# Kernel optimization log

Measured on AMD Instinct MI355X. Metric: run time of the kernel, lower is better.

## Reference

```python
import jax, jax.numpy as jnp
import numpy as np

B, N = 8, 2048
DIN, DH, DE = 32, 64, 64
R = 3          # number_relations
L = 3          # num_layers -> 1 first + 1 block + 1 last
PRED_IN = DH * (L - 1) + DE  # concat: 64*2 + 64 = 192
EPS_BN = 1e-5
EPS_NORM = 1e-12


def setup_inputs() -> dict:
    key = jax.random.key(0)
    ks = jax.random.split(key, 12)
    x = jax.random.normal(ks[0], (B, N, DIN), jnp.float32)
    # relation labels in {0..R}; 0 = no edge, 1..R = relation type
    relation = jax.random.randint(ks[1], (B, N, N), 0, R + 1).astype(jnp.int32)
    # adjacency is the 0/1 edge indicator (float), as the torch code treats it
    adj = (relation > 0).astype(jnp.float32)
    s = 0.05
    w_first = jax.random.normal(ks[2], (R, DIN, DH), jnp.float32) * s
    b_first = jnp.zeros((DH,), jnp.float32)
    w_block = jax.random.normal(ks[3], (R, DH, DH), jnp.float32) * s
    b_block = jnp.zeros((DH,), jnp.float32)
    w_last = jax.random.normal(ks[4], (R, DH, DE), jnp.float32) * s
    b_last = jnp.zeros((DE,), jnp.float32)
    w_map = jax.random.normal(ks[5], (PRED_IN, DE), jnp.float32) * s
    b_map = jnp.zeros((DE,), jnp.float32)
    return {"x": x, "relation": relation, "adj": adj,
            "w_first": w_first, "b_first": b_first,
            "w_block": w_block, "b_block": b_block,
            "w_last": w_last, "b_last": b_last,
            "w_map": w_map, "b_map": b_map}


def _graph_conv(x, rel, W, b):
    # rel: [B,N,N] (int labels or float adjacency); W: [R, din, dout]
    y = jnp.zeros((x.shape[0], x.shape[1], W.shape[2]), x.dtype)
    for i in range(R):  # fixed, small relation count
        mask = (rel == (i + 1)).astype(x.dtype)            # [B,N,N]
        h = jnp.einsum('bij,bjd->bid', mask, x)            # masked aggregation
        y = y + jnp.einsum('bid,de->bie', h, W[i])
    y = y + b
    # F.normalize(p=2, dim=2): v / max(||v||, eps)
    nrm = jnp.sqrt(jnp.sum(y * y, axis=2, keepdims=True))
    return y / jnp.maximum(nrm, EPS_NORM)


def _apply_bn(x):
    # fresh BatchNorm1d(N) in training mode, affine weight=1/bias=0:
    # normalize over (batch, feature) per node index, biased variance
    mean = jnp.mean(x, axis=(0, 2), keepdims=True)
    var = jnp.mean(jnp.square(x - mean), axis=(0, 2), keepdims=True)
    return (x - mean) * jax.lax.rsqrt(var + EPS_BN)


def reference(x, relation, adj, w_first, b_first, w_block, b_block,
              w_last, b_last, w_map, b_map):
    # conv_first uses `relation`
    h = _apply_bn(jax.nn.relu(_graph_conv(x, relation, w_first, b_first)))
    out_all = [jnp.max(h, axis=1)]
    # conv_block and conv_last are (faithfully) called with `adj` as relation
    h = _apply_bn(jax.nn.relu(_graph_conv(h, adj, w_block, b_block)))
    out_all.append(jnp.max(h, axis=1))
    h = _graph_conv(h, adj, w_last, b_last)
    out_all.append(jnp.max(h, axis=1))
    output = jnp.concatenate(out_all, axis=1)        # [B, PRED_IN]
    ypred = output @ w_map + b_map                   # map_model Linear
    return (output, ypred)
```

## Files before the change

### kernel.cpp

```cpp
#include <hip/hip_runtime.h>


#define NN 2048
#define PLANE_W 1048576L

typedef short short8 __attribute__((ext_vector_type(8)));
typedef float floatx4 __attribute__((ext_vector_type(4)));

__device__ __forceinline__ unsigned short f2bf(float x) {
  unsigned u = __float_as_uint(x);
  u += 0x7FFFu + ((u >> 16) & 1u);
  return (unsigned short)(u >> 16);
}

__device__ void dev_xw_first(char* smemc, int u, int tid,
                             const float* __restrict__ x,
                             const float* __restrict__ w,
                             unsigned short* __restrict__ xws) {
  float* xs = (float*)smemc;
  float* wsh = (float*)(smemc + 64 * 33 * 4);
  const int jc = u & 31, b = (u >> 5) & 7, r = u >> 8;
  const int j0 = jc * 64;
  for (int idx = tid; idx < 64 * 32; idx += 256) {
    int row = idx >> 5, f = idx & 31;
    xs[row * 33 + f] = x[((long)b * NN + j0 + row) * 32 + f];
    wsh[idx] = w[r * 2048 + idx];
  }
  __syncthreads();
  const int j = tid & 63, g = tid >> 6;
  const int k = j0 + j;
  const int kblk = k >> 5, kq = (k >> 3) & 3, kj = k & 7;
  unsigned short* dst =
      xws + (((long)(r * 8 + b) * 64 + kblk) * 4 + g) * 512 + kj;
  float xr[32];
#pragma unroll
  for (int f = 0; f < 32; ++f) xr[f] = xs[j * 33 + f];
#pragma unroll
  for (int ii = 0; ii < 16; ++ii) {
    float acc = 0.f;
#pragma unroll
    for (int f = 0; f < 32; ++f) acc += xr[f] * wsh[f * 64 + g * 16 + ii];
    dst[(kq * 16 + ii) * 8] = f2bf(acc);
  }
  __syncthreads();
}

__global__ __launch_bounds__(256) void k_pack_xw1(const int* __restrict__ rel,
                                                  unsigned* __restrict__ planes,
                                                  const float* __restrict__ x,
                                                  const float* __restrict__ w,
                                                  unsigned short* __restrict__ xws) {
  __shared__ __align__(16) char smem[16640];
  const int bid = blockIdx.x, tid = threadIdx.x;
  if (bid < 768) dev_xw_first(smem, bid, tid, x, w, xws);
  for (long t = (long)bid * 256 + tid; t < 1048576L; t += 4096L * 256) {
    int w32 = (int)(t & 63);
    long bi = t >> 6;
    const int4* rp = (const int4*)(rel + bi * NN + w32 * 32);
    unsigned m0 = 0, m1 = 0, m2 = 0;
#pragma unroll
    for (int c = 0; c < 8; ++c) {
      int4 v = rp[c];
      int vv[4] = {v.x, v.y, v.z, v.w};
#pragma unroll
      for (int j = 0; j < 4; ++j) {
        unsigned b1 = 1u << (c * 4 + j);
        m0 |= (vv[j] == 1) ? b1 : 0u;
        m1 |= (vv[j] == 2) ? b1 : 0u;
        m2 |= (vv[j] == 3) ? b1 : 0u;
      }
    }
    long o = bi * 64 + w32;
    planes[o] = m0;
    planes[PLANE_W + o] = m1;
    planes[2 * PLANE_W + o] = m2;
    planes[3 * PLANE_W + o] = m0 | m1 | m2;
  }
}

template <int NREL, bool RELU, bool POOL3>
__global__ __launch_bounds__(512) void k_gemm8(
    const unsigned* __restrict__ planes, const unsigned short* __restrict__ xws,
    const float* __restrict__ bias, float* __restrict__ Hout,
    float* __restrict__ part3) {
  constexpr int MASK_BYTES = NREL * 8448;
  __shared__ __align__(16) char smem[65536];
  unsigned* mw = (unsigned*)smem;
  uint2* lut = (uint2*)(smem + MASK_BYTES);
  floatx4* cb = (floatx4*)smem;
  const int bid = blockIdx.x;
  const int b = bid & 7, it = bid >> 3;
  const int tid = threadIdx.x;
  const int wave = tid >> 6, lane = tid & 63;
  const int m = lane & 15, kq = lane >> 4;
  const unsigned shamt = kq * 8;
  const int i0 = it * 64;

  if (tid < 16) {
    unsigned n = tid;
    lut[n] = make_uint2(((n & 1u) ? 0x3f80u : 0u) | ((n & 2u) ? 0x3f800000u : 0u),
                        ((n & 4u) ? 0x3f80u : 0u) | ((n & 8u) ? 0x3f800000u : 0u));
  }

  floatx4 acc[4][4];
#pragma unroll
  for (int rs = 0; rs < 4; ++rs)
#pragma unroll
    for (int t = 0; t < 4; ++t) acc[rs][t] = floatx4{0, 0, 0, 0};

  for (int chunk = 0; chunk < 2; ++chunk) {
    for (int idx = tid; idx < NREL * 2048; idx += 512) {
      int p = idx >> 11, rem = idx & 2047, row = rem >> 5, w = rem & 31;
      long g = ((long)b * NN + i0 + row) * 64 + chunk * 32 + w;
      unsigned v;
      if (NREL == 3)
        v = planes[(long)p * PLANE_W + g];
      else
        v = planes[3 * PLANE_W + g];
      mw[(p * 64 + row) * 33 + w] = v;
    }
    __syncthreads();
#pragma unroll
    for (int j = 0; j < 4; ++j) {
      const int kk = j * 8 + wave;
      const int kblk = chunk * 32 + kk;
#pragma unroll
      for (int p = 0; p < NREL; ++p) {
        const unsigned short* bb =
            xws + ((long)(p * 8 + b) * 64 + kblk) * 2048 + lane * 8;
        short8 bf0 = *(const short8*)(bb);
        short8 bf1 = *(const short8*)(bb + 512);
        short8 bf2 = *(const short8*)(bb + 1024);
        short8 bf3 = *(const short8*)(bb + 1536);
#pragma unroll
        for (int rs = 0; rs < 4; ++rs) {
          unsigned word = mw[(p * 64 + rs * 16 + m) * 33 + kk];
          unsigned byte = (word >> shamt) & 0xffu;
          uint2 lo = lut[byte & 15u];
          uint2 hi = lut[byte >> 4];
          union {
            unsigned uu[4];
            short8 s8;
          } fr;
          fr.uu[0] = lo.x;
          fr.uu[1] = lo.y;
          fr.uu[2] = hi.x;
          fr.uu[3] = hi.y;
          acc[rs][0] = __builtin_amdgcn_mfma_f32_16x16x32_bf16(fr.s8, bf0,
                                                              acc[rs][0], 0, 0, 0);
          acc[rs][1] = __builtin_amdgcn_mfma_f32_16x16x32_bf16(fr.s8, bf1,
                                                              acc[rs][1], 0, 0, 0);
          acc[rs][2] = __builtin_amdgcn_mfma_f32_16x16x32_bf16(fr.s8, bf2,
                                                              acc[rs][2], 0, 0, 0);
          acc[rs][3] = __builtin_amdgcn_mfma_f32_16x16x32_bf16(fr.s8, bf3,
                                                              acc[rs][3], 0, 0, 0);
        }
      }
    }
    __syncthreads();
  }

  if (wave >= 4) {
    const int src = wave - 4;
#pragma unroll
    for (int rs = 0; rs < 4; ++rs)
#pragma unroll
      for (int t = 0; t < 4; ++t)
        cb[((rs * 4 + src) * 4 + t) * 64 + lane] = acc[rs][t];
  }
  __syncthreads();
  if (wave < 4) {
#pragma unroll
    for (int rs = 0; rs < 4; ++rs)
#pragma unroll
      for (int t = 0; t < 4; ++t) {
        const int ix = ((rs * 4 + wave) * 4 + t) * 64 + lane;
        cb[ix] = cb[ix] + acc[rs][t];
      }
  }
  __syncthreads();
  if (wave < 4) {
    const int rs = wave;
    floatx4 s[4];
#pragma unroll
    for (int t = 0; t < 4; ++t) s[t] = cb[((rs * 4 + 0) * 4 + t) * 64 + lane];
#pragma unroll
    for (int src = 1; src < 4; ++src)
#pragma unroll
      for (int t = 0; t < 4; ++t)
        s[t] += cb[((rs * 4 + src) * 4 + t) * 64 + lane];
    float bv[4];
#pragma unroll
    for (int t = 0; t < 4; ++t) bv[t] = bias[t * 16 + m];
    float pmt[4] = {-3.4e38f, -3.4e38f, -3.4e38f, -3.4e38f};
#pragma unroll
    for (int reg = 0; reg < 4; ++reg) {
#pragma unroll
      for (int t = 0; t < 4; ++t) s[t][reg] += bv[t];
      float q = s[0][reg] * s[0][reg] + s[1][reg] * s[1][reg] +
                s[2][reg] * s[2][reg] + s[3][reg] * s[3][reg];
#pragma unroll
      for (int off = 1; off <= 8; off <<= 1) q += __shfl_xor(q, off);
      q = 1.0f / fmaxf(sqrtf(q), 1e-12f);
#pragma unroll
      for (int t = 0; t < 4; ++t) {
        float o = s[t][reg] * q;
        if (RELU) o = fmaxf(o, 0.0f);
        if (POOL3)
          pmt[t] = fmaxf(pmt[t], o);
        else
          Hout[((long)b * NN + i0 + rs * 16 + kq * 4 + reg) * 64 + t * 16 + m] = o;
      }
    }
    if (POOL3) {
#pragma unroll
      for (int t = 0; t < 4; ++t) {
        pmt[t] = fmaxf(pmt[t], __shfl_xor(pmt[t], 16));
        pmt[t] = fmaxf(pmt[t], __shfl_xor(pmt[t], 32));
      }
      float* pm = (float*)(smem + wave * 16384);
      if (kq == 0) {
#pragma unroll
        for (int t = 0; t < 4; ++t) pm[t * 16 + m] = pmt[t];
      }
    }
  }
  if (POOL3) {
    __syncthreads();
    if (tid < 64) {
      float v = -3.4e38f;
#pragma unroll
      for (int w = 0; w < 4; ++w)
        v = fmaxf(v, ((const float*)(smem + w * 16384))[tid]);
      part3[((long)b * 32 + it) * 64 + tid] = v;
    }
  }
}

__global__ __launch_bounds__(256) void k_xwh_bn(const float* __restrict__ H,
                                                const float* __restrict__ w,
                                                unsigned short* __restrict__ xws,
                                                float* __restrict__ PP) {
  __shared__ float hs[64 * 65];
  __shared__ float wsh[64 * 64];
  __shared__ float sm[64], srs[64];
  const int bid = blockIdx.x, tid = threadIdx.x;
  const int jc = bid & 31, b = bid >> 5;
  const int j0 = jc * 64;
  {
    const int n = tid >> 2, q = tid & 3;
    float s1 = 0.f, s2 = 0.f;
#pragma unroll
    for (int bb = 0; bb < 8; ++bb) {
      const float4* hp =
          (const float4*)(H + ((long)bb * NN + j0 + n) * 64 + q * 16);
#pragma unroll
      for (int c = 0; c < 4; ++c) {
        float4 v = hp[c];
        s1 += v.x + v.y + v.z + v.w;
        s2 += v.x * v.x + v.y * v.y + v.z * v.z + v.w * v.w;
      }
    }
    s1 += __shfl_xor(s1, 1);
    s2 += __shfl_xor(s2, 1);
    s1 += __shfl_xor(s1, 2);
    s2 += __shfl_xor(s2, 2);
    if (q == 0) {
      float mean = s1 * (1.0f / 512.0f);
      float var = fmaxf(s2 * (1.0f / 512.0f) - mean * mean, 0.0f);
      sm[n] = mean;
      srs[n] = rsqrtf(var + 1e-5f);
    }
  }
  __syncthreads();
  for (int idx = tid; idx < 4096; idx += 256) {
    int row = idx >> 6, f = idx & 63;
    float v = H[((long)b * NN + j0 + row) * 64 + f];
    hs[row * 65 + f] = (v - sm[row]) * srs[row];
    wsh[idx] = w[idx];
  }
  __syncthreads();
  {
    const int j = tid & 63, g = tid >> 6;
    const int k = j0 + j;
    const int kblk = k >> 5, kq = (k >> 3) & 3, kj = k & 7;
    unsigned short* dst = xws + (((long)b * 64 + kblk) * 4 + g) * 512 + kj;
    float acc[16];
#pragma unroll
    for (int ii = 0; ii < 16; ++ii) acc[ii] = 0.f;
#pragma unroll
    for (int c = 0; c < 4; ++c) {
      float xr[16];
#pragma unroll
      for (int f = 0; f < 16; ++f) xr[f] = hs[j * 65 + c * 16 + f];
#pragma unroll
      for (int ii = 0; ii < 16; ++ii)
#pragma unroll
        for (int f = 0; f < 16; ++f)
          acc[ii] += xr[f] * wsh[(c * 16 + f) * 64 + g * 16 + ii];
    }
#pragma unroll
    for (int ii = 0; ii < 16; ++ii) dst[(kq * 16 + ii) * 8] = f2bf(acc[ii]);
  }
  if (b == 0) {
#pragma unroll
    for (int part = 0; part < 2; ++part) {
      const int col = part * 256 + tid;
      const int bb = col >> 6, e = col & 63;
      float mx = -3.4e38f;
      for (int n = 0; n < 64; ++n) {
        float v = H[((long)bb * NN + j0 + n) * 64 + e];
        mx = fmaxf(mx, (v - sm[n]) * srs[n]);
      }
      PP[(long)jc * 512 + col] = mx;
    }
  }
}

__global__ __launch_bounds__(512) void k_tail(const float* __restrict__ PP1,
                                              const float* __restrict__ PP2,
                                              const float* __restrict__ P3,
                                              float* __restrict__ out,
                                              const float* __restrict__ wmap,
                                              const float* __restrict__ bmap) {
  __shared__ float obuf[8 * 192];
  const int col = threadIdx.x;
  const int bb = col >> 6, e = col & 63;
  float m1 = -3.4e38f, m2 = -3.4e38f, m3 = -3.4e38f;
#pragma unroll
  for (int c = 0; c < 32; ++c) {
    m1 = fmaxf(m1, PP1[(long)c * 512 + col]);
    m2 = fmaxf(m2, PP2[(long)c * 512 + col]);
    m3 = fmaxf(m3, P3[((long)bb * 32 + c) * 64 + e]);
  }
  out[bb * 192 + e] = m1;
  out[bb * 192 + 64 + e] = m2;
  out[bb * 192 + 128 + e] = m3;
  obuf[bb * 192 + e] = m1;
  obuf[bb * 192 + 64 + e] = m2;
  obuf[bb * 192 + 128 + e] = m3;
  __syncthreads();
  float acc = bmap[e];
#pragma unroll 4
  for (int k = 0; k < 192; ++k) acc += obuf[bb * 192 + k] * wmap[k * 64 + e];
  out[1536 + bb * 64 + e] = acc;
}

extern "C" void kernel_launch(void* const* d_in, const int* in_sizes, int n_in,
                              void* d_out, int out_size, void* d_ws,
                              size_t ws_size, hipStream_t stream) {
  const float* x = (const float*)d_in[0];
  const int* rel = (const int*)d_in[1];
  const float* w_first = (const float*)d_in[3];
  const float* b_first = (const float*)d_in[4];
  const float* w_block = (const float*)d_in[5];
  const float* b_block = (const float*)d_in[6];
  const float* w_last = (const float*)d_in[7];
  const float* b_last = (const float*)d_in[8];
  const float* w_map = (const float*)d_in[9];
  const float* b_map = (const float*)d_in[10];
  float* out = (float*)d_out;

  char* ws = (char*)d_ws;
  const size_t MB = 1024 * 1024;
  unsigned* PLANES = (unsigned*)(ws);
  unsigned short* XWS = (unsigned short*)(ws + 16 * MB);
  float* H = (float*)(ws + 22 * MB);
  float* PP1 = (float*)(ws + 26 * MB);
  float* PP2 = (float*)(ws + 27 * MB);
  float* PART3 = (float*)(ws + 28 * MB);

  k_pack_xw1<<<4096, 256, 0, stream>>>(rel, PLANES, x, w_first, XWS);
  k_gemm8<3, true, false><<<256, 512, 0, stream>>>(PLANES, XWS, b_first, H,
                                                   nullptr);
  k_xwh_bn<<<256, 256, 0, stream>>>(H, w_block, XWS, PP1);
  k_gemm8<1, true, false><<<256, 512, 0, stream>>>(PLANES, XWS, b_block, H,
                                                   nullptr);
  k_xwh_bn<<<256, 256, 0, stream>>>(H, w_last, XWS, PP2);
  k_gemm8<1, false, true><<<256, 512, 0, stream>>>(PLANES, XWS, b_last,
                                                   nullptr, PART3);
  k_tail<<<1, 512, 0, stream>>>(PP1, PP2, PART3, out, w_map, b_map);
}
```

Baseline: 355.8 us.

## Load full mask rows once, remap K order, fuse tail into last GEMM

The relation-plane packing now has each wave read a contiguous 1024-int half-row, emitting 16-bit masks, with a matching permuted K ordering (kvirt) applied to the XW operand layout. The GEMM loads the whole 2048-wide mask tile into shared memory once instead of in two chunks, which removes one barrier pair per chunk. The separate tail kernel is folded into the last GEMM through an atomic completion counter, so the final block does the pooling and the linear map. This saves a launch and gives coalesced relation reads, at the cost of more shared memory per block (possible occupancy loss) and a last-block serialization.

```diff
diff --git a/kernel.cpp b/kernel.cpp
--- a/kernel.cpp
+++ b/kernel.cpp
@@ -11,6 +11,12 @@
   unsigned u = __float_as_uint(x);
   u += 0x7FFFu + ((u >> 16) & 1u);
   return (unsigned short)(u >> 16);
+}
+
+__device__ __forceinline__ int kvirt(int k) {
+  const int chunk = k >> 10, kin = k & 1023;
+  return chunk * 1024 + ((kin >> 2) & 63) * 16 + ((kin >> 8) & 3) * 4 +
+         (kin & 3);
 }
 
 __device__ void dev_xw_first(char* smemc, int u, int tid,
@@ -28,8 +34,8 @@
   }
   __syncthreads();
   const int j = tid & 63, g = tid >> 6;
-  const int k = j0 + j;
-  const int kblk = k >> 5, kq = (k >> 3) & 3, kj = k & 7;
+  const int V = kvirt(j0 + j);
+  const int kblk = V >> 5, kq = (V >> 3) & 3, kj = V & 7;
   unsigned short* dst =
       xws + (((long)(r * 8 + b) * 64 + kblk) * 4 + g) * 512 + kj;
   float xr[32];
@@ -45,36 +51,119 @@
   __syncthreads();
 }
 
-__global__ __launch_bounds__(256) void k_pack_xw1(const int* __restrict__ rel,
-                                                  unsigned* __restrict__ planes,
-                                                  const float* __restrict__ x,
-                                                  const float* __restrict__ w,
-                                                  unsigned short* __restrict__ xws) {
-  __shared__ __align__(16) char smem[16640];
+__global__ __launch_bounds__(256) void k_pack_xw1(
+    const int* __restrict__ rel, unsigned* __restrict__ planes,
+    const float* __restrict__ x, const float* __restrict__ w,
+    unsigned short* __restrict__ xws, unsigned* __restrict__ done) {
+  __shared__ __align__(16) char smemc[16640];
   const int bid = blockIdx.x, tid = threadIdx.x;
-  if (bid < 768) dev_xw_first(smem, bid, tid, x, w, xws);
-  for (long t = (long)bid * 256 + tid; t < 1048576L; t += 4096L * 256) {
-    int w32 = (int)(t & 63);
-    long bi = t >> 6;
-    const int4* rp = (const int4*)(rel + bi * NN + w32 * 32);
+  if (bid == 0 && tid == 0) *done = 0u;
+  if (bid < 768) dev_xw_first(smemc, bid, tid, x, w, xws);
+  unsigned short* ph = (unsigned short*)planes;
+  const int wave = tid >> 6, lane = tid & 63;
+  const int gwid = bid * 4 + wave;
+#pragma unroll
+  for (int s = 0; s < 2; ++s) {
+    const int u = gwid * 2 + s;
+    const int chunk = u & 1;
+    const long bi = u >> 1;
+    const int4* rp = (const int4*)(rel + bi * NN + chunk * 1024);
+    int4 v[4];
+#pragma unroll
+    for (int c = 0; c < 4; ++c) v[c] = rp[c * 64 + lane];
     unsigned m0 = 0, m1 = 0, m2 = 0;
 #pragma unroll
-    for (int c = 0; c < 8; ++c) {
-      int4 v = rp[c];
-      int vv[4] = {v.x, v.y, v.z, v.w};
+    for (int c = 0; c < 4; ++c) {
+      int vv[4] = {v[c].x, v[c].y, v[c].z, v[c].w};
 #pragma unroll
       for (int j = 0; j < 4; ++j) {
-        unsigned b1 = 1u << (c * 4 + j);
-        m0 |= (vv[j] == 1) ? b1 : 0u;
-        m1 |= (vv[j] == 2) ? b1 : 0u;
-        m2 |= (vv[j] == 3) ? b1 : 0u;
-      }
-    }
-    long o = bi * 64 + w32;
-    planes[o] = m0;
-    planes[PLANE_W + o] = m1;
-    planes[2 * PLANE_W + o] = m2;
-    planes[3 * PLANE_W + o] = m0 | m1 | m2;
+        unsigned bit = 1u << (c * 4 + j);
+        m0 |= (vv[j] == 1) ? bit : 0u;
+        m1 |= (vv[j] == 2) ? bit : 0u;
+        m2 |= (vv[j] == 3) ? bit : 0u;
+      }
+    }
+    const long h = (bi * 64 + chunk * 32) * 2 + lane;
+    ph[h] = (unsigned short)m0;
+    ph[2 * PLANE_W + h] = (unsigned short)m1;
+    ph[4 * PLANE_W + h] = (unsigned short)m2;
+    ph[6 * PLANE_W + h] = (unsigned short)(m0 | m1 | m2);
+  }
+}
+
+template <bool RELU, bool POOL3>
+__device__ __forceinline__ void gemm_epilogue(
+    char* smem, int b, int it, int tid, floatx4 (&acc)[4][4],
+    const float* __restrict__ bias, float* __restrict__ Hout) {
+  floatx4* cb = (floatx4*)smem;
+  const int wave = tid >> 6, lane = tid & 63;
+  const int m = lane & 15, kq = lane >> 4;
+  const int i0 = it * 64;
+  if (wave >= 4) {
+    const int src = wave - 4;
+#pragma unroll
+    for (int rs = 0; rs < 4; ++rs)
+#pragma unroll
+      for (int t = 0; t < 4; ++t)
+        cb[((rs * 4 + src) * 4 + t) * 64 + lane] = acc[rs][t];
+  }
+  __syncthreads();
+  if (wave < 4) {
+#pragma unroll
+    for (int rs = 0; rs < 4; ++rs)
+#pragma unroll
+      for (int t = 0; t < 4; ++t) {
+        const int ix = ((rs * 4 + wave) * 4 + t) * 64 + lane;
+        cb[ix] = cb[ix] + acc[rs][t];
+      }
+  }
+  __syncthreads();
+  if (wave < 4) {
+    const int rs = wave;
+    floatx4 s[4];
+#pragma unroll
+    for (int t = 0; t < 4; ++t) s[t] = cb[((rs * 4 + 0) * 4 + t) * 64 + lane];
+#pragma unroll
+    for (int src = 1; src < 4; ++src)
+#pragma unroll
+      for (int t = 0; t < 4; ++t)
+        s[t] += cb[((rs * 4 + src) * 4 + t) * 64 + lane];
+    float bv[4];
+#pragma unroll
+    for (int t = 0; t < 4; ++t) bv[t] = bias[t * 16 + m];
+    float pmt[4] = {-3.4e38f, -3.4e38f, -3.4e38f, -3.4e38f};
+#pragma unroll
+    for (int reg = 0; reg < 4; ++reg) {
+#pragma unroll
+      for (int t = 0; t < 4; ++t) s[t][reg] += bv[t];
+      float q = s[0][reg] * s[0][reg] + s[1][reg] * s[1][reg] +
+                s[2][reg] * s[2][reg] + s[3][reg] * s[3][reg];
+#pragma unroll
+      for (int off = 1; off <= 8; off <<= 1) q += __shfl_xor(q, off);
+      q = 1.0f / fmaxf(sqrtf(q), 1e-12f);
+#pragma unroll
+      for (int t = 0; t < 4; ++t) {
+        float o = s[t][reg] * q;
+        if (RELU) o = fmaxf(o, 0.0f);
+        if (POOL3)
+          pmt[t] = fmaxf(pmt[t], o);
+        else
+          Hout[((long)b * NN + i0 + rs * 16 + kq * 4 + reg) * 64 + t * 16 +
+               m] = o;
+      }
+    }
+    if (POOL3) {
+#pragma unroll
+      for (int t = 0; t < 4; ++t) {
+        pmt[t] = fmaxf(pmt[t], __shfl_xor(pmt[t], 16));
+        pmt[t] = fmaxf(pmt[t], __shfl_xor(pmt[t], 32));
+      }
+      float* pm = (float*)(smem + wave * 16384);
+      if (kq == 0) {
+#pragma unroll
+        for (int t = 0; t < 4; ++t) pm[t * 16 + m] = pmt[t];
+      }
+    }
   }
 }
 
@@ -82,12 +171,14 @@
 __global__ __launch_bounds__(512) void k_gemm8(
     const unsigned* __restrict__ planes, const unsigned short* __restrict__ xws,
     const float* __restrict__ bias, float* __restrict__ Hout,
-    float* __restrict__ part3) {
-  constexpr int MASK_BYTES = NREL * 8448;
+    float* __restrict__ part3, const float* __restrict__ PP1,
+    const float* __restrict__ PP2, float* __restrict__ out,
+    const float* __restrict__ wmap, const float* __restrict__ bmap,
+    unsigned* __restrict__ done) {
   __shared__ __align__(16) char smem[65536];
+  __shared__ int s_last;
   unsigned* mw = (unsigned*)smem;
-  uint2* lut = (uint2*)(smem + MASK_BYTES);
-  floatx4* cb = (floatx4*)smem;
+  uint2* lut = (uint2*)(smem + NREL * 16896);
   const int bid = blockIdx.x;
   const int b = bid & 7, it = bid >> 3;
   const int tid = threadIdx.x;
@@ -98,8 +189,9 @@
 
   if (tid < 16) {
     unsigned n = tid;
-    lut[n] = make_uint2(((n & 1u) ? 0x3f80u : 0u) | ((n & 2u) ? 0x3f800000u : 0u),
-                        ((n & 4u) ? 0x3f80u : 0u) | ((n & 8u) ? 0x3f800000u : 0u));
+    lut[n] =
+        make_uint2(((n & 1u) ? 0x3f80u : 0u) | ((n & 2u) ? 0x3f800000u : 0u),
+                   ((n & 4u) ? 0x3f80u : 0u) | ((n & 8u) ? 0x3f800000u : 0u));
   }
 
   floatx4 acc[4][4];
@@ -108,123 +200,57 @@
 #pragma unroll
     for (int t = 0; t < 4; ++t) acc[rs][t] = floatx4{0, 0, 0, 0};
 
-  for (int chunk = 0; chunk < 2; ++chunk) {
-    for (int idx = tid; idx < NREL * 2048; idx += 512) {
-      int p = idx >> 11, rem = idx & 2047, row = rem >> 5, w = rem & 31;
-      long g = ((long)b * NN + i0 + row) * 64 + chunk * 32 + w;
-      unsigned v;
-      if (NREL == 3)
-        v = planes[(long)p * PLANE_W + g];
-      else
-        v = planes[3 * PLANE_W + g];
-      mw[(p * 64 + row) * 33 + w] = v;
-    }
-    __syncthreads();
-#pragma unroll
-    for (int j = 0; j < 4; ++j) {
-      const int kk = j * 8 + wave;
-      const int kblk = chunk * 32 + kk;
-#pragma unroll
-      for (int p = 0; p < NREL; ++p) {
-        const unsigned short* bb =
-            xws + ((long)(p * 8 + b) * 64 + kblk) * 2048 + lane * 8;
-        short8 bf0 = *(const short8*)(bb);
-        short8 bf1 = *(const short8*)(bb + 512);
-        short8 bf2 = *(const short8*)(bb + 1024);
-        short8 bf3 = *(const short8*)(bb + 1536);
-#pragma unroll
-        for (int rs = 0; rs < 4; ++rs) {
-          unsigned word = mw[(p * 64 + rs * 16 + m) * 33 + kk];
-          unsigned byte = (word >> shamt) & 0xffu;
-          uint2 lo = lut[byte & 15u];
-          uint2 hi = lut[byte >> 4];
-          union {
-            unsigned uu[4];
-            short8 s8;
-          } fr;
-          fr.uu[0] = lo.x;
-          fr.uu[1] = lo.y;
-          fr.uu[2] = hi.x;
-          fr.uu[3] = hi.y;
-          acc[rs][0] = __builtin_amdgcn_mfma_f32_16x16x32_bf16(fr.s8, bf0,
-                                                              acc[rs][0], 0, 0, 0);
-          acc[rs][1] = __builtin_amdgcn_mfma_f32_16x16x32_bf16(fr.s8, bf1,
-                                                              acc[rs][1], 0, 0, 0);
-          acc[rs][2] = __builtin_amdgcn_mfma_f32_16x16x32_bf16(fr.s8, bf2,
-                                                              acc[rs][2], 0, 0, 0);
-          acc[rs][3] = __builtin_amdgcn_mfma_f32_16x16x32_bf16(fr.s8, bf3,
-                                                              acc[rs][3], 0, 0, 0);
-        }
-      }
-    }
-    __syncthreads();
-  }
-
-  if (wave >= 4) {
-    const int src = wave - 4;
-#pragma unroll
-    for (int rs = 0; rs < 4; ++rs)
-#pragma unroll
-      for (int t = 0; t < 4; ++t)
-        cb[((rs * 4 + src) * 4 + t) * 64 + lane] = acc[rs][t];
-  }
-  __syncthreads();
-  if (wave < 4) {
-#pragma unroll
-    for (int rs = 0; rs < 4; ++rs)
-#pragma unroll
-      for (int t = 0; t < 4; ++t) {
-        const int ix = ((rs * 4 + wave) * 4 + t) * 64 + lane;
-        cb[ix] = cb[ix] + acc[rs][t];
-      }
-  }
-  __syncthreads();
-  if (wave < 4) {
-    const int rs = wave;
-    floatx4 s[4];
-#pragma unroll
-    for (int t = 0; t < 4; ++t) s[t] = cb[((rs * 4 + 0) * 4 + t) * 64 + lane];
-#pragma unroll
-    for (int src = 1; src < 4; ++src)
-#pragma unroll
-      for (int t = 0; t < 4; ++t)
-        s[t] += cb[((rs * 4 + src) * 4 + t) * 64 + lane];
-    float bv[4];
-#pragma unroll
-    for (int t = 0; t < 4; ++t) bv[t] = bias[t * 16 + m];
-    float pmt[4] = {-3.4e38f, -3.4e38f, -3.4e38f, -3.4e38f};
-#pragma unroll
-    for (int reg = 0; reg < 4; ++reg) {
-#pragma unroll
-      for (int t = 0; t < 4; ++t) s[t][reg] += bv[t];
-      float q = s[0][reg] * s[0][reg] + s[1][reg] * s[1][reg] +
-                s[2][reg] * s[2][reg] + s[3][reg] * s[3][reg];
-#pragma unroll
-      for (int off = 1; off <= 8; off <<= 1) q += __shfl_xor(q, off);
-      q = 1.0f / fmaxf(sqrtf(q), 1e-12f);
-#pragma unroll
-      for (int t = 0; t < 4; ++t) {
-        float o = s[t][reg] * q;
-        if (RELU) o = fmaxf(o, 0.0f);
-        if (POOL3)
-          pmt[t] = fmaxf(pmt[t], o);
-        else
-          Hout[((long)b * NN + i0 + rs * 16 + kq * 4 + reg) * 64 + t * 16 + m] = o;
-      }
-    }
-    if (POOL3) {
-#pragma unroll
-      for (int t = 0; t < 4; ++t) {
-        pmt[t] = fmaxf(pmt[t], __shfl_xor(pmt[t], 16));
-        pmt[t] = fmaxf(pmt[t], __shfl_xor(pmt[t], 32));
-      }
-      float* pm = (float*)(smem + wave * 16384);
-      if (kq == 0) {
-#pragma unroll
-        for (int t = 0; t < 4; ++t) pm[t * 16 + m] = pmt[t];
-      }
-    }
-  }
+  for (int idx = tid; idx < NREL * 4096; idx += 512) {
+    const int p = idx >> 12, rem = idx & 4095, row = rem >> 6, w = rem & 63;
+    const long g = ((long)b * NN + i0 + row) * 64 + w;
+    unsigned v;
+    if (NREL == 3)
+      v = planes[(long)p * PLANE_W + g];
+    else
+      v = planes[3 * PLANE_W + g];
+    mw[(p * 64 + row) * 66 + w] = v;
+  }
+  __syncthreads();
+
+#pragma unroll 2
+  for (int j = 0; j < 8; ++j) {
+    const int kblk = j * 8 + wave;
+#pragma unroll
+    for (int p = 0; p < NREL; ++p) {
+      const unsigned short* bb =
+          xws + ((long)(p * 8 + b) * 64 + kblk) * 2048 + lane * 8;
+      short8 bf0 = *(const short8*)(bb);
+      short8 bf1 = *(const short8*)(bb + 512);
+      short8 bf2 = *(const short8*)(bb + 1024);
+      short8 bf3 = *(const short8*)(bb + 1536);
+#pragma unroll
+      for (int rs = 0; rs < 4; ++rs) {
+        unsigned word = mw[(p * 64 + rs * 16 + m) * 66 + kblk];
+        unsigned byte = (word >> shamt) & 0xffu;
+        uint2 lo = lut[byte & 15u];
+        uint2 hi = lut[byte >> 4];
+        union {
+          unsigned uu[4];
+          short8 s8;
+        } fr;
+        fr.uu[0] = lo.x;
+        fr.uu[1] = lo.y;
+        fr.uu[2] = hi.x;
+        fr.uu[3] = hi.y;
+        acc[rs][0] = __builtin_amdgcn_mfma_f32_16x16x32_bf16(fr.s8, bf0,
+                                                             acc[rs][0], 0, 0, 0);
+        acc[rs][1] = __builtin_amdgcn_mfma_f32_16x16x32_bf16(fr.s8, bf1,
+                                                             acc[rs][1], 0, 0, 0);
+        acc[rs][2] = __builtin_amdgcn_mfma_f32_16x16x32_bf16(fr.s8, bf2,
+                                                             acc[rs][2], 0, 0, 0);
+        acc[rs][3] = __builtin_amdgcn_mfma_f32_16x16x32_bf16(fr.s8, bf3,
+                                                             acc[rs][3], 0, 0, 0);
+      }
+    }
+  }
+  __syncthreads();
+  gemm_epilogue<RELU, POOL3>(smem, b, it, tid, acc, bias, Hout);
+
   if (POOL3) {
     __syncthreads();
     if (tid < 64) {
@@ -233,6 +259,34 @@
       for (int w = 0; w < 4; ++w)
         v = fmaxf(v, ((const float*)(smem + w * 16384))[tid]);
       part3[((long)b * 32 + it) * 64 + tid] = v;
+    }
+    __threadfence();
+    __syncthreads();
+    if (tid == 0) s_last = (atomicAdd(done, 1u) == 255u) ? 1 : 0;
+    __syncthreads();
+    if (s_last) {
+      __threadfence();
+      float* obuf = (float*)smem;
+      const int col = tid;
+      const int bb = col >> 6, e = col & 63;
+      float m1 = -3.4e38f, m2 = -3.4e38f, m3 = -3.4e38f;
+#pragma unroll
+      for (int c = 0; c < 32; ++c) {
+        m1 = fmaxf(m1, PP1[(long)c * 512 + col]);
+        m2 = fmaxf(m2, PP2[(long)c * 512 + col]);
+        m3 = fmaxf(m3, part3[((long)bb * 32 + c) * 64 + e]);
+      }
+      out[bb * 192 + e] = m1;
+      out[bb * 192 + 64 + e] = m2;
+      out[bb * 192 + 128 + e] = m3;
+      obuf[bb * 192 + e] = m1;
+      obuf[bb * 192 + 64 + e] = m2;
+      obuf[bb * 192 + 128 + e] = m3;
+      __syncthreads();
+      float a = bmap[e];
+#pragma unroll 4
+      for (int k = 0; k < 192; ++k) a += obuf[bb * 192 + k] * wmap[k * 64 + e];
+      out[1536 + bb * 64 + e] = a;
     }
   }
 }
@@ -282,8 +336,8 @@
   __syncthreads();
   {
     const int j = tid & 63, g = tid >> 6;
-    const int k = j0 + j;
-    const int kblk = k >> 5, kq = (k >> 3) & 3, kj = k & 7;
+    const int V = kvirt(j0 + j);
+    const int kblk = V >> 5, kq = (V >> 3) & 3, kj = V & 7;
     unsigned short* dst = xws + (((long)b * 64 + kblk) * 4 + g) * 512 + kj;
     float acc[16];
 #pragma unroll
@@ -315,35 +369,6 @@
       PP[(long)jc * 512 + col] = mx;
     }
   }
-}
-
-__global__ __launch_bounds__(512) void k_tail(const float* __restrict__ PP1,
-                                              const float* __restrict__ PP2,
-                                              const float* __restrict__ P3,
-                                              float* __restrict__ out,
-                                              const float* __restrict__ wmap,
-                                              const float* __restrict__ bmap) {
-  __shared__ float obuf[8 * 192];
-  const int col = threadIdx.x;
-  const int bb = col >> 6, e = col & 63;
-  float m1 = -3.4e38f, m2 = -3.4e38f, m3 = -3.4e38f;
-#pragma unroll
-  for (int c = 0; c < 32; ++c) {
-    m1 = fmaxf(m1, PP1[(long)c * 512 + col]);
-    m2 = fmaxf(m2, PP2[(long)c * 512 + col]);
-    m3 = fmaxf(m3, P3[((long)bb * 32 + c) * 64 + e]);
-  }
-  out[bb * 192 + e] = m1;
-  out[bb * 192 + 64 + e] = m2;
-  out[bb * 192 + 128 + e] = m3;
-  obuf[bb * 192 + e] = m1;
-  obuf[bb * 192 + 64 + e] = m2;
-  obuf[bb * 192 + 128 + e] = m3;
-  __syncthreads();
-  float acc = bmap[e];
-#pragma unroll 4
-  for (int k = 0; k < 192; ++k) acc += obuf[bb * 192 + k] * wmap[k * 64 + e];
-  out[1536 + bb * 64 + e] = acc;
 }
 
 extern "C" void kernel_launch(void* const* d_in, const int* in_sizes, int n_in,
@@ -369,15 +394,17 @@
   float* PP1 = (float*)(ws + 26 * MB);
   float* PP2 = (float*)(ws + 27 * MB);
   float* PART3 = (float*)(ws + 28 * MB);
-
-  k_pack_xw1<<<4096, 256, 0, stream>>>(rel, PLANES, x, w_first, XWS);
-  k_gemm8<3, true, false><<<256, 512, 0, stream>>>(PLANES, XWS, b_first, H,
-                                                   nullptr);
+  unsigned* DONE = (unsigned*)(ws + 29 * MB);
+
+  k_pack_xw1<<<4096, 256, 0, stream>>>(rel, PLANES, x, w_first, XWS, DONE);
+  k_gemm8<3, true, false><<<256, 512, 0, stream>>>(
+      PLANES, XWS, b_first, H, nullptr, nullptr, nullptr, nullptr, nullptr,
+      nullptr, nullptr);
   k_xwh_bn<<<256, 256, 0, stream>>>(H, w_block, XWS, PP1);
-  k_gemm8<1, true, false><<<256, 512, 0, stream>>>(PLANES, XWS, b_block, H,
-                                                   nullptr);
+  k_gemm8<1, true, false><<<256, 512, 0, stream>>>(
+      PLANES, XWS, b_block, H, nullptr, nullptr, nullptr, nullptr, nullptr,
+      nullptr, nullptr);
   k_xwh_bn<<<256, 256, 0, stream>>>(H, w_last, XWS, PP2);
-  k_gemm8<1, false, true><<<256, 512, 0, stream>>>(PLANES, XWS, b_last,
-                                                   nullptr, PART3);
-  k_tail<<<1, 512, 0, stream>>>(PP1, PP2, PART3, out, w_map, b_map);
-}
+  k_gemm8<1, false, true><<<256, 512, 0, stream>>>(
+      PLANES, XWS, b_last, nullptr, PART3, PP1, PP2, out, w_map, b_map, DONE);
+}
```

Result: slower. 384.5 us (+8.1%).
